# Kernel tuning notes

Measured on AMD Instinct MI355X. Metric: run time of the kernel, lower is better.

Reference implementation:

```python
import jax, jax.numpy as jnp
import numpy as np
from jax import lax


def _binarize(w):
    # XNOR-style sign binarization: sign(w) with sign(0) -> +1
    return jnp.where(w >= 0, 1.0, -1.0).astype(w.dtype)


def setup_inputs() -> dict:
    key = jax.random.key(0)
    kx, kw = jax.random.split(key)
    X = jax.random.normal(kx, (32, 256, 56, 56), dtype=jnp.float32)   # NCHW
    W = jax.random.normal(kw, (256, 256, 3, 3), dtype=jnp.float32)    # OIHW
    return {"X": X, "W": W}


def reference(X, W):
    Wb = _binarize(W)
    # F.conv2d default: padding=0 (VALID), stride=1
    out = lax.conv_general_dilated(
        X, Wb,
        window_strides=(1, 1),
        padding="VALID",
        dimension_numbers=("NCHW", "OIHW", "NCHW"),
    )
    return out  # [32, 256, 54, 54]
```

## Files before the change

kernel.cpp:

```cpp
#include <hip/hip_runtime.h>
#include <stdint.h>

typedef float f32x4 __attribute__((ext_vector_type(4)));
typedef __bf16 bf16x8 __attribute__((ext_vector_type(8)));
typedef unsigned short u16x8 __attribute__((ext_vector_type(8)));

#define NIMG 32
#define CIN  256
#define HIN  56
#define WIN  56
#define HWIN 3136
#define COUT 256
#define HOUT 54
#define WOUT 54
#define HWOUT 2916
#define NPOS 93312

#define XT_BYTES   ((size_t)NIMG*HWIN*CIN*2)
#define WT_OFF     (XT_BYTES + 8192)
#define WT_BYTES   ((size_t)9*8*256*32*2)
#define WS_NEED    (WT_OFF + WT_BYTES)

static __device__ __forceinline__ unsigned short f2bf(float f) {
    union { float f; uint32_t u; } v; v.f = f;
    return (unsigned short)((v.u + 0x7FFFu + ((v.u >> 16) & 1u)) >> 16);
}

static __device__ __forceinline__ void gload16(const void* g, void* l) {
    __builtin_amdgcn_global_load_lds(
        (const __attribute__((address_space(1))) void*)g,
        (__attribute__((address_space(3))) void*)l, 16, 0, 0);
}

__global__ void wxform(const float* __restrict__ W, unsigned short* __restrict__ Wt) {
    int idx = blockIdx.x * 256 + threadIdx.x;
    int cb = idx & 31;
    int o  = (idx >> 5) & 255;
    int cc = (idx >> 13) & 7;
    int k  = idx >> 16;
    int c  = cc * 32 + cb;
    float w = W[(size_t)(o * 256 + c) * 9 + k];
    Wt[idx] = (w >= 0.0f) ? (unsigned short)0x3F80 : (unsigned short)0xBF80;
}

__global__ void xxform(const float* __restrict__ X, unsigned short* __restrict__ Xt) {
    __shared__ float tile[32][65];
    int bid = blockIdx.x;
    int hwc = bid % 49;
    int cc  = (bid / 49) & 7;
    int n   = bid / (49 * 8);
    int hw0 = hwc * 64;
    int c0  = cc * 32;
    int t = threadIdx.x;
    {
        int c = t >> 3;
        int w = (t & 7) * 8;
        const float* src = X + (size_t)(n * CIN + c0 + c) * HWIN + hw0 + w;
        float4 a = *(const float4*)src;
        float4 b = *(const float4*)(src + 4);
        tile[c][w + 0] = a.x; tile[c][w + 1] = a.y; tile[c][w + 2] = a.z; tile[c][w + 3] = a.w;
        tile[c][w + 4] = b.x; tile[c][w + 5] = b.y; tile[c][w + 6] = b.z; tile[c][w + 7] = b.w;
    }
    __syncthreads();
    {
        int w  = t >> 2;
        int cb = (t & 3) * 8;
        u16x8 v;
        #pragma unroll
        for (int j = 0; j < 8; ++j) v[j] = f2bf(tile[cb + j][w]);
        *(u16x8*)(Xt + (size_t)(n * HWIN + hw0 + w) * 256 + c0 + cb) = v;
    }
}

__global__ __launch_bounds__(128, 2)
void bconv_gemm(const unsigned short* __restrict__ Xt,
                const unsigned short* __restrict__ Wt,
                float* __restrict__ out) {
    __shared__ __align__(16) unsigned short lds[4096 + 2048];
    const int t    = threadIdx.x;
    const int wid  = t >> 6;
    const int lane = t & 63;
    const int l15  = lane & 15;
    const int lg   = lane >> 4;
    const uint32_t P0 = blockIdx.x * 64u;
    const int o0 = blockIdx.y * 128;

    const int cb16 = (t & 3) * 8;
    uint32_t base0[2];
    #pragma unroll
    for (int r = 0; r < 2; ++r) {
        uint32_t P  = P0 + (t >> 2) + r * 32;
        uint32_t n  = P / (uint32_t)HWOUT;
        uint32_t rm = P - n * HWOUT;
        uint32_t ph = rm / 54u;
        uint32_t pw = rm - ph * 54u;
        base0[r] = n * HWIN + ph * 56u + pw;
    }

    f32x4 acc[4][4];
    #pragma unroll
    for (int m = 0; m < 4; ++m)
        #pragma unroll
        for (int nn = 0; nn < 4; ++nn)
            acc[m][nn] = (f32x4){0.f, 0.f, 0.f, 0.f};

    uint32_t aoff[4], boff[4];
    #pragma unroll
    for (int m = 0; m < 4; ++m)  aoff[m] = (uint32_t)((wid * 64 + m * 16 + l15) * 32 + lg * 8);
    #pragma unroll
    for (int nn = 0; nn < 4; ++nn) boff[nn] = (uint32_t)(4096 + (nn * 16 + l15) * 32 + lg * 8);

    for (int kh = 0; kh < 3; ++kh) {
        for (int c0 = 0; c0 < 8; ++c0) {
            #pragma unroll
            for (int kw = 0; kw < 3; ++kw) {
                const int k9 = kh * 3 + kw;
                const unsigned short* aG = Wt + (size_t)(k9 * 8 + c0) * 8192 + o0 * 32 + t * 8;
                #pragma unroll
                for (int r = 0; r < 4; ++r)
                    gload16(aG + r * 1024, (unsigned short*)lds + r * 1024 + t * 8);
                const uint32_t khw = (uint32_t)(kh * 56 + kw);
                #pragma unroll
                for (int r = 0; r < 2; ++r) {
                    const unsigned short* bG = Xt + ((size_t)(base0[r] + khw)) * 256 + c0 * 32 + cb16;
                    gload16(bG, (unsigned short*)lds + 4096 + r * 1024 + t * 8);
                }
                __syncthreads();
                bf16x8 af[4], bfr[4];
                #pragma unroll
                for (int m = 0; m < 4; ++m)
                    af[m] = __builtin_bit_cast(bf16x8, *(const u16x8*)(lds + aoff[m]));
                #pragma unroll
                for (int nn = 0; nn < 4; ++nn)
                    bfr[nn] = __builtin_bit_cast(bf16x8, *(const u16x8*)(lds + boff[nn]));
                #pragma unroll
                for (int m = 0; m < 4; ++m)
                    #pragma unroll
                    for (int nn = 0; nn < 4; ++nn)
                        acc[m][nn] = __builtin_amdgcn_mfma_f32_16x16x32_bf16(
                            af[m], bfr[nn], acc[m][nn], 0, 0, 0);
                __syncthreads();
            }
        }
    }

    #pragma unroll
    for (int nn = 0; nn < 4; ++nn) {
        uint32_t P  = P0 + nn * 16 + l15;
        uint32_t n  = P / (uint32_t)HWOUT;
        uint32_t rm = P - n * HWOUT;
        float* obase = out + (size_t)(n * 256u + o0 + wid * 64) * HWOUT + rm;
        #pragma unroll
        for (int m = 0; m < 4; ++m)
            #pragma unroll
            for (int r = 0; r < 4; ++r)
                obase[(size_t)(m * 16 + lg * 4 + r) * HWOUT] = acc[m][nn][r];
    }
}

__global__ void bconv_fallback(const float* __restrict__ X, const float* __restrict__ W,
                               float* __restrict__ out) {
    size_t idx = (size_t)blockIdx.x * 256 + threadIdx.x;
    int ow = (int)(idx % 54);
    int oh = (int)((idx / 54) % 54);
    int o  = (int)((idx / 2916) % 256);
    int n  = (int)(idx / 746496);
    float s = 0.f;
    for (int c = 0; c < 256; ++c) {
        const float* xr = X + ((size_t)(n * 256 + c) * 56 + oh) * 56 + ow;
        const float* wr = W + (size_t)(o * 256 + c) * 9;
        #pragma unroll
        for (int kh = 0; kh < 3; ++kh)
            #pragma unroll
            for (int kw = 0; kw < 3; ++kw) {
                float w = wr[kh * 3 + kw];
                float x = xr[kh * 56 + kw];
                s += (w >= 0.f) ? x : -x;
            }
    }
    out[idx] = s;
}

extern "C" void kernel_launch(void* const* d_in, const int* in_sizes, int n_in,
                              void* d_out, int out_size, void* d_ws, size_t ws_size,
                              hipStream_t stream) {
    const float* X = (const float*)d_in[0];
    const float* W = (const float*)d_in[1];
    float* out = (float*)d_out;

    if (ws_size < WS_NEED) {
        bconv_fallback<<<93312, 256, 0, stream>>>(X, W, out);
        return;
    }
    unsigned short* Xt = (unsigned short*)d_ws;
    unsigned short* Wt = (unsigned short*)((char*)d_ws + WT_OFF);

    wxform<<<2304, 256, 0, stream>>>(W, Wt);
    xxform<<<12544, 256, 0, stream>>>(X, Xt);

    dim3 grid(1458, 2);
    bconv_gemm<<<grid, 128, 0, stream>>>(Xt, Wt, out);
}
```

Baseline: 171.1 us.

## Rewrite binary conv GEMM with 256x128 tiles, double-buffered LDS pipeline, swizzled layout

The GEMM kernel moves from 128-thread blocks with 128x64 tiles and single-buffered 32-wide K steps to 512-thread blocks with 128x256 tiles and 64-wide K steps. Global-to-LDS loads are double-buffered and prefetched two steps ahead, and barriers are interleaved with MFMA groups and s_setprio so loads overlap compute. LDS uses an XOR swizzle to avoid bank conflicts, and the weight layout is reordered to match. The intent is to hide memory latency and raise data reuse per LDS byte. In exchange it uses 96KB of LDS and hand-placed waitcnts, which are fragile and limit occupancy.

```diff
diff --git a/kernel.cpp b/kernel.cpp
--- a/kernel.cpp
+++ b/kernel.cpp
@@ -7,18 +7,14 @@
 
 #define NIMG 32
 #define CIN  256
-#define HIN  56
-#define WIN  56
 #define HWIN 3136
 #define COUT 256
-#define HOUT 54
-#define WOUT 54
 #define HWOUT 2916
 #define NPOS 93312
 
 #define XT_BYTES   ((size_t)NIMG*HWIN*CIN*2)
 #define WT_OFF     (XT_BYTES + 8192)
-#define WT_BYTES   ((size_t)9*8*256*32*2)
+#define WT_BYTES   ((size_t)9*4*2*128*64*2)
 #define WS_NEED    (WT_OFF + WT_BYTES)
 
 static __device__ __forceinline__ unsigned short f2bf(float f) {
@@ -32,14 +28,48 @@
         (__attribute__((address_space(3))) void*)l, 16, 0, 0);
 }
 
+static __device__ __forceinline__ uint32_t lds_a(const void* p) {
+    return (uint32_t)(uintptr_t)(__attribute__((address_space(3))) const void*)p;
+}
+
+static __device__ __forceinline__ u16x8 ldsr(uint32_t addr) {
+    u16x8 r;
+    asm volatile("ds_read_b128 %0, %1" : "=v"(r) : "v"(addr));
+    return r;
+}
+
+#define BAR()   __builtin_amdgcn_s_barrier()
+#define LGKM0() do { asm volatile("s_waitcnt lgkmcnt(0)" ::: "memory"); \
+                     __builtin_amdgcn_sched_barrier(0); } while (0)
+#define VM2()   asm volatile("s_waitcnt vmcnt(2)" ::: "memory")
+#define VM6()   asm volatile("s_waitcnt vmcnt(6)" ::: "memory")
+#define VM0()   asm volatile("s_waitcnt vmcnt(0)" ::: "memory")
+#define PRIO1() __builtin_amdgcn_s_setprio(1)
+#define PRIO0() __builtin_amdgcn_s_setprio(0)
+
+#define MF(a_, b_, c_) __builtin_amdgcn_mfma_f32_16x16x32_bf16( \
+    __builtin_bit_cast(bf16x8, a_), __builtin_bit_cast(bf16x8, b_), c_, 0, 0, 0)
+
+#define QUAD(aa, ab, m0_, m1_, c0_, c1_, c2_, c3_)         \
+    acc[m0_][0] = MF(aa, c0_, acc[m0_][0]);                \
+    acc[m0_][1] = MF(aa, c1_, acc[m0_][1]);                \
+    acc[m0_][2] = MF(aa, c2_, acc[m0_][2]);                \
+    acc[m0_][3] = MF(aa, c3_, acc[m0_][3]);                \
+    acc[m1_][0] = MF(ab, c0_, acc[m1_][0]);                \
+    acc[m1_][1] = MF(ab, c1_, acc[m1_][1]);                \
+    acc[m1_][2] = MF(ab, c2_, acc[m1_][2]);                \
+    acc[m1_][3] = MF(ab, c3_, acc[m1_][3]);
+
 __global__ void wxform(const float* __restrict__ W, unsigned short* __restrict__ Wt) {
     int idx = blockIdx.x * 256 + threadIdx.x;
-    int cb = idx & 31;
-    int o  = (idx >> 5) & 255;
-    int cc = (idx >> 13) & 7;
-    int k  = idx >> 16;
-    int c  = cc * 32 + cb;
-    float w = W[(size_t)(o * 256 + c) * 9 + k];
+    int c6 = idx & 63;
+    int o7 = (idx >> 6) & 127;
+    int ob = (idx >> 13) & 1;
+    int cc = (idx >> 14) & 3;
+    int k9 = idx >> 16;
+    int o = ob * 128 + o7;
+    int c = cc * 64 + c6;
+    float w = W[(size_t)(o * 256 + c) * 9 + k9];
     Wt[idx] = (w >= 0.0f) ? (unsigned short)0x3F80 : (unsigned short)0xBF80;
 }
 
@@ -72,89 +102,155 @@
     }
 }
 
-__global__ __launch_bounds__(128, 2)
+__global__ __launch_bounds__(512, 2)
 void bconv_gemm(const unsigned short* __restrict__ Xt,
                 const unsigned short* __restrict__ Wt,
                 float* __restrict__ out) {
-    __shared__ __align__(16) unsigned short lds[4096 + 2048];
+    __shared__ __align__(16) char smem[98304];
+
     const int t    = threadIdx.x;
     const int wid  = t >> 6;
     const int lane = t & 63;
     const int l15  = lane & 15;
     const int lg   = lane >> 4;
-    const uint32_t P0 = blockIdx.x * 64u;
-    const int o0 = blockIdx.y * 128;
-
-    const int cb16 = (t & 3) * 8;
-    uint32_t base0[2];
+    const int wr   = wid >> 2;
+    const int wc   = wid & 3;
+    const int ob   = blockIdx.x;
+    const uint32_t P0 = blockIdx.y * 256u;
+
+    const uint32_t colx = (uint32_t)(((t & 7) ^ ((t >> 3) & 7)) << 3);
+    const uint32_t aG   = (uint32_t)(t >> 3) * 64u + colx;
+
+    uint32_t base0[4];
     #pragma unroll
-    for (int r = 0; r < 2; ++r) {
-        uint32_t P  = P0 + (t >> 2) + r * 32;
-        uint32_t n  = P / (uint32_t)HWOUT;
-        uint32_t rm = P - n * HWOUT;
+    for (int r = 0; r < 4; ++r) {
+        uint32_t pos = P0 + (uint32_t)(r * 64 + (t >> 3));
+        if (pos >= NPOS) pos = NPOS - 1;
+        uint32_t ni = pos / (uint32_t)HWOUT;
+        uint32_t rm = pos - ni * HWOUT;
         uint32_t ph = rm / 54u;
         uint32_t pw = rm - ph * 54u;
-        base0[r] = n * HWIN + ph * 56u + pw;
-    }
+        base0[r] = ni * HWIN + ph * 56u + pw;
+    }
+
+    const uint32_t x7  = (uint32_t)(l15 & 7);
+    const uint32_t ck0 = ((((uint32_t)lg) ^ x7) << 4);
+    const uint32_t ck1 = (((4u | (uint32_t)lg) ^ x7) << 4);
+    const uint32_t ar0 = (uint32_t)(wr * 64 + 0 * 16 + l15) * 128u;
+    const uint32_t ar1 = (uint32_t)(wr * 64 + 1 * 16 + l15) * 128u;
+    const uint32_t ar2 = (uint32_t)(wr * 64 + 2 * 16 + l15) * 128u;
+    const uint32_t ar3 = (uint32_t)(wr * 64 + 3 * 16 + l15) * 128u;
+    const uint32_t br0 = 16384u + (uint32_t)(wc * 64 + 0 * 16 + l15) * 128u;
+    const uint32_t br1 = 16384u + (uint32_t)(wc * 64 + 1 * 16 + l15) * 128u;
+    const uint32_t br2 = 16384u + (uint32_t)(wc * 64 + 2 * 16 + l15) * 128u;
+    const uint32_t br3 = 16384u + (uint32_t)(wc * 64 + 3 * 16 + l15) * 128u;
+
+    const uint32_t E = lds_a(smem);
+    const uint32_t O = E + 49152u;
 
     f32x4 acc[4][4];
     #pragma unroll
     for (int m = 0; m < 4; ++m)
         #pragma unroll
-        for (int nn = 0; nn < 4; ++nn)
-            acc[m][nn] = (f32x4){0.f, 0.f, 0.f, 0.f};
-
-    uint32_t aoff[4], boff[4];
+        for (int n = 0; n < 4; ++n)
+            acc[m][n] = (f32x4){0.f, 0.f, 0.f, 0.f};
+
+    auto STAGE_A = [&](uint32_t bufoff, int kt) {
+        int k9 = kt >> 2, cc = kt & 3;
+        const unsigned short* p = Wt + ((size_t)(((k9 << 2) | cc) * 2 + ob)) * 8192 + aG;
+        gload16(p,        smem + bufoff + (size_t)t * 16);
+        gload16(p + 4096, smem + bufoff + 8192 + (size_t)t * 16);
+    };
+    auto STAGE_B2 = [&](uint32_t bufoff, int kt, int r0) {
+        int k9 = kt >> 2, cc = kt & 3;
+        int kh = k9 / 3, kw = k9 - kh * 3;
+        uint32_t khw = (uint32_t)(kh * 56 + kw);
+        #pragma unroll
+        for (int r = r0; r < r0 + 2; ++r) {
+            const unsigned short* p = Xt + (size_t)(base0[r] + khw) * 256 + (uint32_t)cc * 64u + colx;
+            gload16(p, smem + bufoff + 16384 + (size_t)r * 8192 + (size_t)t * 16);
+        }
+    };
+
+    STAGE_A(0, 0);      STAGE_B2(0, 0, 0);      STAGE_B2(0, 0, 2);
+    STAGE_A(49152u, 1); STAGE_B2(49152u, 1, 0); STAGE_B2(49152u, 1, 2);
+    VM6();
+    BAR();
+
+    u16x8 a00, a01, a10, a11;
+    u16x8 b00, b10, b20, b30, b01, b11, b21, b31;
+
+    auto ITER = [&](int kt, bool pf) {
+        a00 = ldsr(E + ar0 + ck0); a01 = ldsr(E + ar0 + ck1);
+        a10 = ldsr(E + ar1 + ck0); a11 = ldsr(E + ar1 + ck1);
+        b00 = ldsr(E + br0 + ck0); b10 = ldsr(E + br1 + ck0);
+        b20 = ldsr(E + br2 + ck0); b30 = ldsr(E + br3 + ck0);
+        BAR(); LGKM0(); PRIO1();
+        QUAD(a00, a10, 0, 1, b00, b10, b20, b30);
+        PRIO0(); BAR();
+        b01 = ldsr(E + br0 + ck1); b11 = ldsr(E + br1 + ck1);
+        b21 = ldsr(E + br2 + ck1); b31 = ldsr(E + br3 + ck1);
+        BAR(); LGKM0(); PRIO1();
+        QUAD(a01, a11, 0, 1, b01, b11, b21, b31);
+        PRIO0(); BAR();
+        a00 = ldsr(E + ar2 + ck0); a01 = ldsr(E + ar2 + ck1);
+        a10 = ldsr(E + ar3 + ck0); a11 = ldsr(E + ar3 + ck1);
+        BAR(); LGKM0(); PRIO1();
+        QUAD(a00, a10, 2, 3, b00, b10, b20, b30);
+        PRIO0(); BAR();
+        if (pf) { STAGE_A(0, kt + 2); VM2(); } else { VM0(); }
+        BAR(); PRIO1();
+        QUAD(a01, a11, 2, 3, b01, b11, b21, b31);
+        PRIO0(); BAR();
+        a00 = ldsr(O + ar0 + ck0); a01 = ldsr(O + ar0 + ck1);
+        a10 = ldsr(O + ar1 + ck0); a11 = ldsr(O + ar1 + ck1);
+        b00 = ldsr(O + br0 + ck0); b10 = ldsr(O + br1 + ck0);
+        b20 = ldsr(O + br2 + ck0); b30 = ldsr(O + br3 + ck0);
+        if (pf) STAGE_B2(0, kt + 2, 0);
+        BAR(); LGKM0(); PRIO1();
+        QUAD(a00, a10, 0, 1, b00, b10, b20, b30);
+        PRIO0(); BAR();
+        b01 = ldsr(O + br0 + ck1); b11 = ldsr(O + br1 + ck1);
+        b21 = ldsr(O + br2 + ck1); b31 = ldsr(O + br3 + ck1);
+        if (pf) STAGE_B2(0, kt + 2, 2);
+        BAR(); LGKM0(); PRIO1();
+        QUAD(a01, a11, 0, 1, b01, b11, b21, b31);
+        PRIO0(); BAR();
+        a00 = ldsr(O + ar2 + ck0); a01 = ldsr(O + ar2 + ck1);
+        a10 = ldsr(O + ar3 + ck0); a11 = ldsr(O + ar3 + ck1);
+        BAR(); LGKM0(); PRIO1();
+        QUAD(a00, a10, 2, 3, b00, b10, b20, b30);
+        PRIO0(); BAR();
+        if (pf) {
+            STAGE_A(49152u, kt + 3);
+            STAGE_B2(49152u, kt + 3, 0);
+            STAGE_B2(49152u, kt + 3, 2);
+            VM6();
+        } else {
+            VM0();
+        }
+        BAR(); PRIO1();
+        QUAD(a01, a11, 2, 3, b01, b11, b21, b31);
+        PRIO0(); BAR();
+    };
+
+    for (int kt = 0; kt < 34; kt += 2) ITER(kt, true);
+    ITER(34, false);
+
+    const int orow0 = ob * 128 + wr * 64;
     #pragma unroll
-    for (int m = 0; m < 4; ++m)  aoff[m] = (uint32_t)((wid * 64 + m * 16 + l15) * 32 + lg * 8);
-    #pragma unroll
-    for (int nn = 0; nn < 4; ++nn) boff[nn] = (uint32_t)(4096 + (nn * 16 + l15) * 32 + lg * 8);
-
-    for (int kh = 0; kh < 3; ++kh) {
-        for (int c0 = 0; c0 < 8; ++c0) {
+    for (int n = 0; n < 4; ++n) {
+        uint32_t P = P0 + (uint32_t)(wc * 64 + n * 16 + l15);
+        if (P < NPOS) {
+            uint32_t ni = P / (uint32_t)HWOUT;
+            uint32_t rm = P - ni * HWOUT;
+            float* ob_ = out + (size_t)(ni * 256u + orow0) * HWOUT + rm;
             #pragma unroll
-            for (int kw = 0; kw < 3; ++kw) {
-                const int k9 = kh * 3 + kw;
-                const unsigned short* aG = Wt + (size_t)(k9 * 8 + c0) * 8192 + o0 * 32 + t * 8;
+            for (int m = 0; m < 4; ++m)
                 #pragma unroll
                 for (int r = 0; r < 4; ++r)
-                    gload16(aG + r * 1024, (unsigned short*)lds + r * 1024 + t * 8);
-                const uint32_t khw = (uint32_t)(kh * 56 + kw);
-                #pragma unroll
-                for (int r = 0; r < 2; ++r) {
-                    const unsigned short* bG = Xt + ((size_t)(base0[r] + khw)) * 256 + c0 * 32 + cb16;
-                    gload16(bG, (unsigned short*)lds + 4096 + r * 1024 + t * 8);
-                }
-                __syncthreads();
-                bf16x8 af[4], bfr[4];
-                #pragma unroll
-                for (int m = 0; m < 4; ++m)
-                    af[m] = __builtin_bit_cast(bf16x8, *(const u16x8*)(lds + aoff[m]));
-                #pragma unroll
-                for (int nn = 0; nn < 4; ++nn)
-                    bfr[nn] = __builtin_bit_cast(bf16x8, *(const u16x8*)(lds + boff[nn]));
-                #pragma unroll
-                for (int m = 0; m < 4; ++m)
-                    #pragma unroll
-                    for (int nn = 0; nn < 4; ++nn)
-                        acc[m][nn] = __builtin_amdgcn_mfma_f32_16x16x32_bf16(
-                            af[m], bfr[nn], acc[m][nn], 0, 0, 0);
-                __syncthreads();
-            }
+                    ob_[(size_t)(m * 16 + lg * 4 + r) * HWOUT] = acc[m][n][r];
         }
-    }
-
-    #pragma unroll
-    for (int nn = 0; nn < 4; ++nn) {
-        uint32_t P  = P0 + nn * 16 + l15;
-        uint32_t n  = P / (uint32_t)HWOUT;
-        uint32_t rm = P - n * HWOUT;
-        float* obase = out + (size_t)(n * 256u + o0 + wid * 64) * HWOUT + rm;
-        #pragma unroll
-        for (int m = 0; m < 4; ++m)
-            #pragma unroll
-            for (int r = 0; r < 4; ++r)
-                obase[(size_t)(m * 16 + lg * 4 + r) * HWOUT] = acc[m][nn][r];
     }
 }
 
@@ -198,6 +294,6 @@
     wxform<<<2304, 256, 0, stream>>>(W, Wt);
     xxform<<<12544, 256, 0, stream>>>(X, Xt);
 
-    dim3 grid(1458, 2);
-    bconv_gemm<<<grid, 128, 0, stream>>>(Xt, Wt, out);
-}
+    dim3 grid(2, 365);
+    bconv_gemm<<<grid, 512, 0, stream>>>(Xt, Wt, out);
+}
```

Result: faster. 163.4 us (-4.5%).
